# Kernel optimization log

Hardware: AMD Instinct MI355X
Metric: run time of the kernel (lower is better)

The kernel has to match this reference:

```python
import jax, jax.numpy as jnp
import numpy as np

EPS = 1e-6
NUM_HEADS = 16


def layer_norm(x, a, b):
    # Faithful to the custom LayerNorm: unbiased std (ddof=1), eps added to sigma.
    mu = jnp.mean(x, axis=-1, keepdims=True)
    sigma = jnp.std(x, axis=-1, keepdims=True, ddof=1) + EPS
    return (x - mu) / sigma * a + b


def entmax15(x):
    # Exact 1.5-entmax along the last axis (Peters et al. 2019, sort-based).
    S = x.shape[-1]
    x = x / 2.0
    x = x - jnp.max(x, axis=-1, keepdims=True)  # shift-invariant stabilization
    xs = jnp.flip(jnp.sort(x, axis=-1), axis=-1)  # descending
    k = jnp.arange(1, S + 1, dtype=x.dtype)
    mean = jnp.cumsum(xs, axis=-1) / k
    meansq = jnp.cumsum(xs * xs, axis=-1) / k
    ss = k * (meansq - mean * mean)
    delta = (1.0 - ss) / k
    tau = mean - jnp.sqrt(jnp.clip(delta, 0.0))
    support_size = jnp.sum((tau <= xs).astype(jnp.int32), axis=-1, keepdims=True)
    tau_star = jnp.take_along_axis(tau, support_size - 1, axis=-1)
    return jnp.clip(x - tau_star, 0.0) ** 2


def linear(x, w, b):
    return jnp.einsum('bsd,od->bso', x, w) + b


def setup_inputs() -> dict:
    key = jax.random.key(0)
    B, S, D, DFF = 1, 2048, 1024, 4096
    ks = jax.random.split(key, 12)
    p = lambda k, shape: jax.random.normal(k, shape, dtype=jnp.float32) * 0.02
    return {
        'inputs': jax.random.normal(ks[0], (B, S, D), dtype=jnp.float32),
        'mask': jax.random.randint(ks[1], (B, S), 0, 2, dtype=jnp.int32),
        'wq': p(ks[2], (D, D)), 'bq': jnp.zeros((D,), jnp.float32),
        'wk': p(ks[3], (D, D)), 'bk': jnp.zeros((D,), jnp.float32),
        'wv': p(ks[4], (D, D)), 'bv': jnp.zeros((D,), jnp.float32),
        'wo': p(ks[5], (D, D)), 'bo': jnp.zeros((D,), jnp.float32),
        'ln1_a': jnp.ones((D,), jnp.float32), 'ln1_b': jnp.zeros((D,), jnp.float32),
        'w1': p(ks[6], (DFF, D)), 'b1': jnp.zeros((DFF,), jnp.float32),
        'w2': p(ks[7], (D, DFF)), 'b2': jnp.zeros((D,), jnp.float32),
        'ln2_a': jnp.ones((D,), jnp.float32), 'ln2_b': jnp.zeros((D,), jnp.float32),
    }


def reference(inputs, mask, wq, bq, wk, bk, wv, bv, wo, bo, ln1_a, ln1_b,
              w1, b1, w2, b2, ln2_a, ln2_b):
    B, S, D = inputs.shape
    H = NUM_HEADS
    hd = D // H

    # --- Sublayer 1: pre-norm -> SparseMHA -> residual (dropout=0 -> identity) ---
    x1 = layer_norm(inputs, ln1_a, ln1_b)
    split = lambda t: t.reshape(B, S, H, hd).transpose(0, 2, 1, 3)  # [B,H,S,hd]
    q = split(linear(x1, wq, bq))
    k = split(linear(x1, wk, bk))
    v = split(linear(x1, wv, bv))

    scores = jnp.einsum('bhqd,bhkd->bhqk', q, k) / jnp.sqrt(jnp.asarray(hd, jnp.float32))
    # torch: mask.unsqueeze(0) -> (1,B,S); with B==1 it broadcasts as a key mask (1,1,1,S)
    mask4 = mask[None, None]  # (1,1,B,S), B==1
    scores = jnp.where(mask4 == 0, jnp.float32(-1e9), scores)

    p_attn = entmax15(scores).astype(jnp.float32)
    attended = jnp.einsum('bhqk,bhkd->bhqd', p_attn, v)
    attended = attended.transpose(0, 2, 1, 3).reshape(B, S, D)
    y = inputs + linear(attended, wo, bo)

    # --- Sublayer 2: pre-norm -> FFN -> residual ---
    x2 = layer_norm(y, ln2_a, ln2_b)
    ffn = linear(jax.nn.relu(linear(x2, w1, b1)), w2, b2)
    return y + ffn
```

## Files before the change

### kernel.cpp

```cpp
#include <hip/hip_runtime.h>
#include <hip/hip_bf16.h>

#define S   2048
#define D   1024
#define DFF 4096
#define NH  16
#define HD  64

typedef unsigned short u16;
typedef unsigned int   u32;
typedef __attribute__((ext_vector_type(8))) short      short8;
typedef __attribute__((ext_vector_type(4))) float      floatx4;
typedef __attribute__((ext_vector_type(2))) _Float16   half2v;
typedef __attribute__((ext_vector_type(4))) _Float16   half4v;
typedef __attribute__((ext_vector_type(8))) _Float16   half8v;

__device__ __forceinline__ float bu2f(u16 u) {
    union { u32 i; float f; } x; x.i = ((u32)u) << 16; return x.f;
}
__device__ __forceinline__ u16 f2bu(float f) {
    __hip_bfloat16 h = __float2bfloat16(f);
    return *(u16*)&h;
}
__device__ __forceinline__ u16 f2h(float f) {
    _Float16 h = (_Float16)f; return *(u16*)&h;
}
__device__ __forceinline__ float ldf(const float* p) { return *p; }
__device__ __forceinline__ float ldf(const u16* p)   { return bu2f(*p); }

__device__ __forceinline__ half2v pkrtz(float a, float b) {
    auto v = __builtin_amdgcn_cvt_pkrtz(a, b);
    union { decltype(v) i; half2v o; } u; u.i = v; return u.o;
}

__device__ __forceinline__ floatx4 mfma_f16(half8v a, half8v b, floatx4 c) {
    return __builtin_amdgcn_mfma_f32_16x16x32_f16(a, b, c, 0, 0, 0);
}
__device__ __forceinline__ float fdot2f(half2v a, half2v b, float c) {
#if __has_builtin(__builtin_amdgcn_fdot2)
    return __builtin_amdgcn_fdot2(a, b, c, false);
#else
    return c + (float)a[0] * (float)b[0] + (float)a[1] * (float)b[1];
#endif
}

template <int K>
__device__ __forceinline__ float ror16f(float v) {
    int s = __builtin_bit_cast(int, v);
    int r = __builtin_amdgcn_update_dpp(s, s, 0x120 | K, 0xF, 0xF, false);
    return __builtin_bit_cast(float, r);
}
__device__ __forceinline__ float rowsum16(float v) {
    v += ror16f<1>(v);
    v += ror16f<2>(v);
    v += ror16f<4>(v);
    v += ror16f<8>(v);
    return v;
}
__device__ __forceinline__ float rowmax16(float v) {
    v = fmaxf(v, ror16f<1>(v));
    v = fmaxf(v, ror16f<2>(v));
    v = fmaxf(v, ror16f<4>(v));
    v = fmaxf(v, ror16f<8>(v));
    return v;
}

__device__ __forceinline__ void async16(const void* g, void* l) {
    __builtin_amdgcn_global_load_lds(
        (const __attribute__((address_space(1))) u32*)g,
        (__attribute__((address_space(3))) u32*)l, 16, 0, 0);
}

#define WAITV(N) asm volatile("s_waitcnt vmcnt(" N ")" ::: "memory")
#define WAITL()  asm volatile("s_waitcnt lgkmcnt(0)" ::: "memory")
#define SBAR()   __builtin_amdgcn_s_barrier()
#define SCHED0() __builtin_amdgcn_sched_barrier(0)

__global__ __launch_bounds__(256)
void cvt_kernel(const float* __restrict__ in, u16* __restrict__ out, int n4)
{
    int i = blockIdx.x * 256 + threadIdx.x;
    if (i < n4) {
        float4 v = ((const float4*)in)[i];
        ushort4 s;
        s.x = f2bu(v.x); s.y = f2bu(v.y); s.z = f2bu(v.z); s.w = f2bu(v.w);
        ((ushort4*)out)[i] = s;
    }
}

__global__ __launch_bounds__(256)
void prep_kernel(const int* __restrict__ mask, int* __restrict__ newpos,
                 int* __restrict__ nkbuf,
                 const float* __restrict__ wq, const float* __restrict__ wk,
                 const float* __restrict__ wv, const float* __restrict__ wo,
                 u16* __restrict__ wqkvb, u16* __restrict__ wob,
                 const float* __restrict__ inp, const float* __restrict__ ln1a,
                 const float* __restrict__ ln1b, u16* __restrict__ x1,
                 const float* __restrict__ w2, u16* __restrict__ w2dst)
{
    const int blk = blockIdx.x;
    const int t = threadIdx.x;
    if (blk == 0) {
        __shared__ int ps[256];
        int loc[8];
        int s = 0;
#pragma unroll
        for (int j = 0; j < 8; j++) {
            loc[j] = s;
            s += (mask[t * 8 + j] != 0);
        }
        ps[t] = s;
        __syncthreads();
        for (int off = 1; off < 256; off <<= 1) {
            int v = (t >= off) ? ps[t - off] : 0;
            __syncthreads();
            ps[t] += v;
            __syncthreads();
        }
        const int total = ps[255];
        const int base = t ? ps[t - 1] : 0;
#pragma unroll
        for (int j = 0; j < 8; j++) {
            const int gi = t * 8 + j;
            const int up = base + loc[j];
            newpos[gi] = mask[gi] ? up : (total + gi - up);
        }
        if (t == 0) nkbuf[0] = total;
    } else if (blk <= 4096) {
        int cb = blk - 1;
        const float* src;
        u16* dst;
        if (cb < 1024)      { src = wq; dst = wqkvb; }
        else if (cb < 2048) { src = wk; dst = wqkvb + 1024 * 1024; cb -= 1024; }
        else if (cb < 3072) { src = wv; dst = wqkvb + 2 * 1024 * 1024; cb -= 2048; }
        else                { src = wo; dst = wob; cb -= 3072; }
        const int i = cb * 256 + t;
        float4 v = ((const float4*)src)[i];
        ushort4 sv;
        sv.x = f2bu(v.x); sv.y = f2bu(v.y); sv.z = f2bu(v.z); sv.w = f2bu(v.w);
        ((ushort4*)dst)[i] = sv;
    } else if (blk <= 6144) {
        const int rrow = blk - 4097;
        const float* x = inp + (size_t)rrow * D;
        float v[4];
        float s = 0.f, ss = 0.f;
#pragma unroll
        for (int j = 0; j < 4; j++) {
            float val = x[t + 256 * j];
            v[j] = val; s += val; ss = fmaf(val, val, ss);
        }
#pragma unroll
        for (int off = 32; off >= 1; off >>= 1) {
            s  += __shfl_down(s,  off, 64);
            ss += __shfl_down(ss, off, 64);
        }
        __shared__ float red[10];
        const int wave = t >> 6, lane = t & 63;
        if (lane == 0) { red[wave] = s; red[4 + wave] = ss; }
        __syncthreads();
        if (t == 0) {
            float S1 = red[0] + red[1] + red[2] + red[3];
            float S2 = red[4] + red[5] + red[6] + red[7];
            float mu = S1 / (float)D;
            float var = (S2 - (float)D * mu * mu) / (float)(D - 1);
            float sig = sqrtf(fmaxf(var, 0.f)) + 1e-6f;
            red[8] = mu; red[9] = 1.f / sig;
        }
        __syncthreads();
        const float mu = red[8], rs = red[9];
#pragma unroll
        for (int j = 0; j < 4; j++) {
            int c = t + 256 * j;
            x1[(size_t)rrow * D + c] = f2bu((v[j] - mu) * rs * ln1a[c] + ln1b[c]);
        }
    } else {
        const int i = (blk - 6145) * 256 + t;
        float4 v = ((const float4*)w2)[i];
        ushort4 sv;
        sv.x = f2bu(v.x); sv.y = f2bu(v.y); sv.z = f2bu(v.z); sv.w = f2bu(v.w);
        ((ushort4*)w2dst)[i] = sv;
    }
}

template <typename T>
__global__ __launch_bounds__(256, 4)
void ln_kernel(const T* __restrict__ in, const float* __restrict__ ga,
               const float* __restrict__ gb, u16* __restrict__ out)
{
    const int row = blockIdx.x;
    const int t = threadIdx.x;
    const T* x = in + (size_t)row * D;
    float v[4];
    float s = 0.f, ss = 0.f;
#pragma unroll
    for (int j = 0; j < 4; j++) {
        float val = ldf(x + t + 256 * j);
        v[j] = val; s += val; ss = fmaf(val, val, ss);
    }
#pragma unroll
    for (int off = 32; off >= 1; off >>= 1) {
        s  += __shfl_down(s,  off, 64);
        ss += __shfl_down(ss, off, 64);
    }
    __shared__ float red[10];
    const int wave = t >> 6, lane = t & 63;
    if (lane == 0) { red[wave] = s; red[4 + wave] = ss; }
    __syncthreads();
    if (t == 0) {
        float S1 = red[0] + red[1] + red[2] + red[3];
        float S2 = red[4] + red[5] + red[6] + red[7];
        float mu = S1 / (float)D;
        float var = (S2 - (float)D * mu * mu) / (float)(D - 1);
        float sig = sqrtf(fmaxf(var, 0.f)) + 1e-6f;
        red[8] = mu; red[9] = 1.f / sig;
    }
    __syncthreads();
    const float mu = red[8], rs = red[9];
#pragma unroll
    for (int j = 0; j < 4; j++) {
        int c = t + 256 * j;
        out[(size_t)row * D + c] = f2bu((v[j] - mu) * rs * ga[c] + gb[c]);
    }
}

#define GEMM_CORE(A_, B_, K_)                                                   \
    __shared__ u16 As[3 * 128 * 32];                                            \
    __shared__ u16 Bs[3 * 128 * 32];                                            \
    const int t = threadIdx.x;                                                  \
    const int w = t >> 6, l = t & 63;                                           \
    const int m0 = blockIdx.y * 128, n0 = blockIdx.x * 128;                     \
    const int qk = l >> 4, col = l & 15;                                        \
    const int wm = (w & 1) * 64, wn = (w >> 1) * 64;                            \
    const int sr  = l >> 2;                                                     \
    const int sq  = l & 3;                                                      \
    const int row = w * 16 + sr;                                                \
    const int gq  = sq ^ ((row >> 1) & 3);                                      \
    const u16* Ap = A_ + (size_t)(m0 + row) * K_ + gq * 8;                      \
    const u16* Bp = B_ + (size_t)(n0 + row) * K_ + gq * 8;                      \
    u16* AsW = As + w * 16 * 32;                                                \
    u16* BsW = Bs + w * 16 * 32;                                                \
    const int mloc = wm + col, nloc = wn + col;                                 \
    const int aoff = mloc * 32 + (qk ^ ((mloc >> 1) & 3)) * 8;                  \
    const int boff = nloc * 32 + (qk ^ ((nloc >> 1) & 3)) * 8;                  \
    floatx4 acc[4][4];                                                          \
    _Pragma("unroll")                                                           \
    for (int i = 0; i < 4; i++)                                                 \
        _Pragma("unroll")                                                       \
        for (int j = 0; j < 4; j++) acc[i][j] = (floatx4)0.f;                   \
    const int NT_ = K_ / 32;                                                    \
    _Pragma("unroll")                                                           \
    for (int s = 0; s < 3; s++) {                                               \
        async16(Ap,                   AsW + s * 4096);                          \
        async16(Ap + (size_t)64 * K_, AsW + s * 4096 + 64 * 32);                \
        async16(Bp,                   BsW + s * 4096);                          \
        async16(Bp + (size_t)64 * K_, BsW + s * 4096 + 64 * 32);                \
        Ap += 32; Bp += 32;                                                     \
    }                                                                           \
    WAITV("8"); SCHED0(); SBAR();                                               \
    int cur = 0;                                                                \
    for (int t0 = 0; t0 + 3 < NT_; ++t0) {                                      \
        short8 a[4], b[4];                                                      \
        const u16* aB = As + cur * 4096 + aoff;                                 \
        const u16* bB = Bs + cur * 4096 + boff;                                 \
        _Pragma("unroll")                                                       \
        for (int i = 0; i < 4; i++) a[i] = *(const short8*)(aB + i * 16 * 32);  \
        _Pragma("unroll")                                                       \
        for (int j = 0; j < 4; j++) b[j] = *(const short8*)(bB + j * 16 * 32);  \
        WAITL(); SCHED0(); SBAR();                                              \
        async16(Ap,                   AsW + cur * 4096);                        \
        async16(Ap + (size_t)64 * K_, AsW + cur * 4096 + 64 * 32);              \
        async16(Bp,                   BsW + cur * 4096);                        \
        async16(Bp + (size_t)64 * K_, BsW + cur * 4096 + 64 * 32);              \
        Ap += 32; Bp += 32;                                                     \
        _Pragma("unroll")                                                       \
        for (int i = 0; i < 4; i++)                                             \
            _Pragma("unroll")                                                   \
            for (int j = 0; j < 4; j++)                                         \
                acc[i][j] = __builtin_amdgcn_mfma_f32_16x16x32_bf16(            \
                    a[i], b[j], acc[i][j], 0, 0, 0);                            \
        WAITV("8"); SCHED0(); SBAR();                                           \
        cur = cur + 1; if (cur == 3) cur = 0;                                   \
    }                                                                           \
    _Pragma("unroll")                                                           \
    for (int tail = 0; tail < 3; tail++) {                                      \
        short8 a[4], b[4];                                                      \
        const u16* aB = As + cur * 4096 + aoff;                                 \
        const u16* bB = Bs + cur * 4096 + boff;                                 \
        _Pragma("unroll")                                                       \
        for (int i = 0; i < 4; i++) a[i] = *(const short8*)(aB + i * 16 * 32);  \
        _Pragma("unroll")                                                       \
        for (int j = 0; j < 4; j++) b[j] = *(const short8*)(bB + j * 16 * 32);  \
        _Pragma("unroll")                                                       \
        for (int i = 0; i < 4; i++)                                             \
            _Pragma("unroll")                                                   \
            for (int j = 0; j < 4; j++)                                         \
                acc[i][j] = __builtin_amdgcn_mfma_f32_16x16x32_bf16(            \
                    a[i], b[j], acc[i][j], 0, 0, 0);                            \
        if (tail == 0) { WAITV("4"); SCHED0(); SBAR(); }                        \
        if (tail == 1) { WAITV("0"); SCHED0(); SBAR(); }                        \
        cur = cur + 1; if (cur == 3) cur = 0;                                   \
    }

template <int OMODE, bool RELU, int RES>
__global__ __launch_bounds__(256, 2)
void gemm_mfma(const u16* __restrict__ A, const u16* __restrict__ B,
               const float* __restrict__ bias, const void* __restrict__ res,
               void* __restrict__ Cout, int M, int N, int K)
{
    GEMM_CORE(A, B, K)
#pragma unroll
    for (int j = 0; j < 4; j++) {
        const int n = n0 + wn + j * 16 + col;
        const float bn = bias[n];
#pragma unroll
        for (int i = 0; i < 4; i++) {
#pragma unroll
            for (int r = 0; r < 4; r++) {
                const int m = m0 + wm + i * 16 + qk * 4 + r;
                float v = acc[i][j][r] + bn;
                if (RELU) v = fmaxf(v, 0.f);
                if (RES == 1) v += ((const float*)res)[(size_t)m * N + n];
                if (RES == 2) v += bu2f(((const u16*)res)[(size_t)m * N + n]);
                if (OMODE == 0) ((float*)Cout)[(size_t)m * N + n] = v;
                if (OMODE == 1) ((u16*)Cout)[(size_t)m * N + n] = f2bu(v);
            }
        }
    }
}

__global__ __launch_bounds__(256, 2)
void gemm_qkv(const u16* __restrict__ A, const u16* __restrict__ B,
              const float* __restrict__ bq, const float* __restrict__ bk,
              const float* __restrict__ bv, const int* __restrict__ np,
              u16* __restrict__ outQ, u16* __restrict__ outK,
              u16* __restrict__ outVT)
{
    const int K = D;
    GEMM_CORE(A, B, K)
    const int seg   = n0 >> 10;
    const int nbase = n0 & 1023;
    const float* bs = (seg == 0) ? bq : (seg == 1) ? bk : bv;
    int npm[4][4];
    if (seg != 0) {
#pragma unroll
        for (int i = 0; i < 4; i++)
#pragma unroll
            for (int r = 0; r < 4; r++)
                npm[i][r] = np[m0 + wm + i * 16 + qk * 4 + r];
    }
#pragma unroll
    for (int j = 0; j < 4; j++) {
        const int nl = nbase + wn + j * 16 + col;
        const float bn = bs[nl];
#pragma unroll
        for (int i = 0; i < 4; i++) {
#pragma unroll
            for (int r = 0; r < 4; r++) {
                const int m = m0 + wm + i * 16 + qk * 4 + r;
                float v = acc[i][j][r] + bn;
                if (seg == 0)      outQ [(size_t)m * D + nl]          = f2h(v);
                else if (seg == 1) outK [(size_t)npm[i][r] * D + nl]  = f2h(v);
                else               outVT[(size_t)nl * S + npm[i][r]]  = f2h(v);
            }
        }
    }
}

template <int OMODE, int RES>
__global__ __launch_bounds__(256, 4)
void gemm64(const u16* __restrict__ A, const u16* __restrict__ B,
            const float* __restrict__ bias, const void* __restrict__ res,
            void* __restrict__ Cout, int M, int N, int K)
{
    __shared__ u16 As[3 * 64 * 32];
    __shared__ u16 Bs[3 * 64 * 32];
    const int t = threadIdx.x;
    const int w = t >> 6, l = t & 63;
    const int m0 = blockIdx.y * 64, n0 = blockIdx.x * 64;
    const int qk = l >> 4, col = l & 15;
    const int wm = (w & 1) * 32, wn = (w >> 1) * 32;
    const int sr = l >> 2, sq = l & 3;
    const int row = w * 16 + sr;
    const int gq = sq ^ ((row >> 1) & 3);
    const u16* Ap = A + (size_t)(m0 + row) * K + gq * 8;
    const u16* Bp = B + (size_t)(n0 + row) * K + gq * 8;
    u16* AsW = As + w * 16 * 32;
    u16* BsW = Bs + w * 16 * 32;
    const int mloc = wm + col, nloc = wn + col;
    const int aoff = mloc * 32 + (qk ^ ((mloc >> 1) & 3)) * 8;
    const int boff = nloc * 32 + (qk ^ ((nloc >> 1) & 3)) * 8;
    floatx4 acc[2][2];
#pragma unroll
    for (int i = 0; i < 2; i++)
#pragma unroll
        for (int j = 0; j < 2; j++) acc[i][j] = (floatx4)0.f;
    const int NT_ = K / 32;
#pragma unroll
    for (int s = 0; s < 3; s++) {
        async16(Ap, AsW + s * 2048);
        async16(Bp, BsW + s * 2048);
        Ap += 32; Bp += 32;
    }
    WAITV("4"); SCHED0(); SBAR();
    int cur = 0;
    for (int t0 = 0; t0 + 3 < NT_; ++t0) {
        short8 a[2], b[2];
        const u16* aB = As + cur * 2048 + aoff;
        const u16* bB = Bs + cur * 2048 + boff;
#pragma unroll
        for (int i = 0; i < 2; i++) a[i] = *(const short8*)(aB + i * 16 * 32);
#pragma unroll
        for (int j = 0; j < 2; j++) b[j] = *(const short8*)(bB + j * 16 * 32);
        WAITL(); SCHED0(); SBAR();
        async16(Ap, AsW + cur * 2048);
        async16(Bp, BsW + cur * 2048);
        Ap += 32; Bp += 32;
#pragma unroll
        for (int i = 0; i < 2; i++)
#pragma unroll
            for (int j = 0; j < 2; j++)
                acc[i][j] = __builtin_amdgcn_mfma_f32_16x16x32_bf16(
                    a[i], b[j], acc[i][j], 0, 0, 0);
        WAITV("4"); SCHED0(); SBAR();
        cur = cur + 1; if (cur == 3) cur = 0;
    }
#pragma unroll
    for (int tail = 0; tail < 3; tail++) {
        short8 a[2], b[2];
        const u16* aB = As + cur * 2048 + aoff;
        const u16* bB = Bs + cur * 2048 + boff;
#pragma unroll
        for (int i = 0; i < 2; i++) a[i] = *(const short8*)(aB + i * 16 * 32);
#pragma unroll
        for (int j = 0; j < 2; j++) b[j] = *(const short8*)(bB + j * 16 * 32);
#pragma unroll
        for (int i = 0; i < 2; i++)
#pragma unroll
            for (int j = 0; j < 2; j++)
                acc[i][j] = __builtin_amdgcn_mfma_f32_16x16x32_bf16(
                    a[i], b[j], acc[i][j], 0, 0, 0);
        if (tail == 0) { WAITV("2"); SCHED0(); SBAR(); }
        if (tail == 1) { WAITV("0"); SCHED0(); SBAR(); }
        cur = cur + 1; if (cur == 3) cur = 0;
    }
#pragma unroll
    for (int j = 0; j < 2; j++) {
        const int n = n0 + wn + j * 16 + col;
        const float bn = bias[n];
#pragma unroll
        for (int i = 0; i < 2; i++) {
#pragma unroll
            for (int r = 0; r < 4; r++) {
                const int m = m0 + wm + i * 16 + qk * 4 + r;
                float v = acc[i][j][r] + bn;
                if (RES == 1) v += ((const float*)res)[(size_t)m * N + n];
                if (RES == 2) v += bu2f(((const u16*)res)[(size_t)m * N + n]);
                if (OMODE == 0) ((float*)Cout)[(size_t)m * N + n] = v;
                if (OMODE == 1) ((u16*)Cout)[(size_t)m * N + n] = f2bu(v);
            }
        }
    }
}

__global__ __launch_bounds__(256, 3)
void attn_cvt(const u16* __restrict__ qb, const u16* __restrict__ kb,
              const u16* __restrict__ vT, const int* __restrict__ nkbuf,
              u16* __restrict__ att,
              const float* __restrict__ w1src, u16* __restrict__ w1dst)
{
    __shared__ u16 Plds[16 * 1024];
    const int blk = blockIdx.x;
    const int t  = threadIdx.x;
    if (blk >= 2048) {
        const int i = (blk - 2048) * 256 + t;
        float4 v = ((const float4*)w1src)[i];
        ushort4 sv;
        sv.x = f2bu(v.x); sv.y = f2bu(v.y); sv.z = f2bu(v.z); sv.w = f2bu(v.w);
        ((ushort4*)w1dst)[i] = sv;
        return;
    }
    const int nk = nkbuf[0];
    const int NS = (nk + 127) >> 7;
    const int NT = (nk + 31) >> 5;
    const int hh = blk >> 7;
    const int q0 = (blk & 127) * 16;
    const int w  = __builtin_amdgcn_readfirstlane(t >> 6);
    const int l  = t & 63;
    const int lg = l >> 4, lc = l & 15;
    const _Float16 NEG = (_Float16)(-30000.f);
    const half4v NEG4 = {NEG, NEG, NEG, NEG};

    const u16* qp = qb + (size_t)(q0 + lc) * D + hh * HD + lg * 8;
    const half8v bq0 = *(const half8v*)qp;
    const half8v bq1 = *(const half8v*)(qp + 32);
    const u16* kbase = kb + hh * HD + lg * 8;
    const int R = 4 * w + lg;
    const half2v one2 = {(_Float16)1.f, (_Float16)1.f};
    const u16* vp = vT + (size_t)(hh * HD + w * 16 + lc) * S + lg * 8;

    if (nk <= 1152) {
#pragma unroll
        for (int T = 0; T < 16; T++) {
            const int g = 4 * T + w;
            if (g < 8 * NS) {
                half4v scv;
                if ((g + 1) * 16 <= nk) {
                    const u16* kp = kbase + (size_t)(g * 16 + lc) * D;
                    floatx4 a = (floatx4)0.f;
                    a = mfma_f16(*(const half8v*)kp,        bq0, a);
                    a = mfma_f16(*(const half8v*)(kp + 32), bq1, a);
                    half2v p01 = pkrtz(a[0] * 0.0625f, a[1] * 0.0625f);
                    half2v p23 = pkrtz(a[2] * 0.0625f, a[3] * 0.0625f);
                    scv = __builtin_shufflevector(p01, p23, 0, 1, 2, 3);
                } else if (g * 16 < nk) {
                    const u16* kp = kbase + (size_t)(g * 16 + lc) * D;
                    floatx4 a = (floatx4)0.f;
                    a = mfma_f16(*(const half8v*)kp,        bq0, a);
                    a = mfma_f16(*(const half8v*)(kp + 32), bq1, a);
                    const int kb0 = g * 16 + lg * 4;
                    half2v p01 = pkrtz(kb0 + 0 < nk ? a[0] * 0.0625f : -30000.f,
                                       kb0 + 1 < nk ? a[1] * 0.0625f : -30000.f);
                    half2v p23 = pkrtz(kb0 + 2 < nk ? a[2] * 0.0625f : -30000.f,
                                       kb0 + 3 < nk ? a[3] * 0.0625f : -30000.f);
                    scv = __builtin_shufflevector(p01, p23, 0, 1, 2, 3);
                } else {
                    scv = NEG4;
                }
                const int kl = g * 16 + lg * 4;
                const int b  = kl >> 3;
                const int p  = b ^ ((b >> 3) & 7) ^ (lc & 7);
                *(half4v*)&Plds[lc * 1024 + p * 8 + (lg & 1) * 4] = scv;
            }
        }
        __syncthreads();

        half8v xq[9];
#pragma unroll
        for (int s = 0; s < 8; s++) {
            if (s < NS) {
                const int b = 16 * s + lc;
                const int p = b ^ ((b >> 3) & 7) ^ (R & 7);
                xq[s] = *(const half8v*)&Plds[R * 1024 + p * 8];
            }
        }
        if (NS > 8) {
            __syncthreads();
#pragma unroll
            for (int T = 16; T < 18; T++) {
                const int g = 4 * T + w;
                half4v scv;
                if ((g + 1) * 16 <= nk) {
                    const u16* kp = kbase + (size_t)(g * 16 + lc) * D;
                    floatx4 a = (floatx4)0.f;
                    a = mfma_f16(*(const half8v*)kp,        bq0, a);
                    a = mfma_f16(*(const half8v*)(kp + 32), bq1, a);
                    half2v p01 = pkrtz(a[0] * 0.0625f, a[1] * 0.0625f);
                    half2v p23 = pkrtz(a[2] * 0.0625f, a[3] * 0.0625f);
                    scv = __builtin_shufflevector(p01, p23, 0, 1, 2, 3);
                } else if (g * 16 < nk) {
                    const u16* kp = kbase + (size_t)(g * 16 + lc) * D;
                    floatx4 a = (floatx4)0.f;
                    a = mfma_f16(*(const half8v*)kp,        bq0, a);
                    a = mfma_f16(*(const half8v*)(kp + 32), bq1, a);
                    const int kb0 = g * 16 + lg * 4;
                    half2v p01 = pkrtz(kb0 + 0 < nk ? a[0] * 0.0625f : -30000.f,
                                       kb0 + 1 < nk ? a[1] * 0.0625f : -30000.f);
                    half2v p23 = pkrtz(kb0 + 2 < nk ? a[2] * 0.0625f : -30000.f,
                                       kb0 + 3 < nk ? a[3] * 0.0625f : -30000.f);
                    scv = __builtin_shufflevector(p01, p23, 0, 1, 2, 3);
                } else {
                    scv = NEG4;
                }
                const int kl = g * 16 + lg * 4 - 1024;
                const int b  = kl >> 3;
                const int p  = b ^ ((b >> 3) & 7) ^ (lc & 7);
                *(half4v*)&Plds[lc * 1024 + p * 8 + (lg & 1) * 4] = scv;
            }
            __syncthreads();
            {
                const int b = lc;
                const int p = b ^ ((b >> 3) & 7) ^ (R & 7);
                xq[8] = *(const half8v*)&Plds[R * 1024 + p * 8];
            }
        }

        float tau;
        {
            half8v m8 = xq[0];
#pragma unroll
            for (int i = 1; i < 9; i++)
                if (i < NS) m8 = __builtin_elementwise_max(m8, xq[i]);
            union { half8v v; half2v h[4]; } u; u.v = m8;
            half2v m2 = __builtin_elementwise_max(
                __builtin_elementwise_max(u.h[0], u.h[1]),
                __builtin_elementwise_max(u.h[2], u.h[3]));
            float mx = fmaxf((float)m2[0], (float)m2[1]);
            mx = rowmax16(mx);
            tau = mx - 1.0f;
        }

        const float nact = (float)(8 * NS);
#pragma unroll 1
        for (int it = 0; it < 12; it++) {
            const _Float16 th = (_Float16)tau;
            const float tf = (float)th;
            const half8v t8 = {th, th, th, th, th, th, th, th};
            float m1a = 0.f, m1b = 0.f, m2a = 0.f, m2b = 0.f;
#pragma unroll
            for (int i = 0; i < 9; i++) {
                if (i < NS) {
                    union { half8v v; half2v h[4]; } u;
                    u.v = __builtin_elementwise_max(xq[i], t8);
                    m1a = fdot2f(u.h[0], one2, m1a);
                    m2a = fdot2f(u.h[0], u.h[0], m2a);
                    m1b = fdot2f(u.h[1], one2, m1b);
                    m2b = fdot2f(u.h[1], u.h[1], m2b);
                    m1a = fdot2f(u.h[2], one2, m1a);
                    m2a = fdot2f(u.h[2], u.h[2], m2a);
                    m1b = fdot2f(u.h[3], one2, m1b);
                    m2b = fdot2f(u.h[3], u.h[3], m2b);
                }
            }
            const float M1 = m1a + m1b, M2 = m2a + m2b;
            float s1 = fmaf(-nact, tf, M1);
            float s2 = fmaf(tf, fmaf(nact, tf, -2.f * M1), M2);
            s1 = rowsum16(s1);
            s2 = rowsum16(s2);
            const float delta = (s2 - 1.0f) / (2.0f * fmaxf(s1, 1e-4f));
            tau += delta;
            if (__all(fabsf(delta) < 2.5e-4f)) break;
        }

        const _Float16 th = (_Float16)tau;
        const half8v t8 = {th, th, th, th, th, th, th, th};
        const half8v z8 = (half8v)(_Float16)0.f;
        floatx4 oa0 = (floatx4)0.f, oa1 = (floatx4)0.f;
        floatx4 oa2 = (floatx4)0.f, oa3 = (floatx4)0.f;
#pragma unroll
        for (int s = 0; s < 8; s++) {
            if (s < NS) {
                half8v dp = __builtin_elementwise_max(xq[s] - t8, z8);
                const int b = 16 * s + lc;
                const int p = b ^ ((b >> 3) & 7) ^ (R & 7);
                *(half8v*)&Plds[R * 1024 + p * 8] = dp * dp;
            }
        }
        __syncthreads();
        __builtin_amdgcn_s_setprio(1);
#pragma unroll
        for (int kt = 0; kt < 32; kt++) {
            if (kt < NT) {
                const int b = kt * 4 + lg;
                const int p = b ^ ((b >> 3) & 7) ^ (lc & 7);
                half8v af = *(const half8v*)&Plds[lc * 1024 + p * 8];
                half8v bf = *(const half8v*)(vp + kt * 32);
                if ((kt & 3) == 0)      oa0 = mfma_f16(af, bf, oa0);
                else if ((kt & 3) == 1) oa1 = mfma_f16(af, bf, oa1);
                else if ((kt & 3) == 2) oa2 = mfma_f16(af, bf, oa2);
                else                    oa3 = mfma_f16(af, bf, oa3);
            }
        }
        __builtin_amdgcn_s_setprio(0);
        if (NS > 8) {
            __syncthreads();
            {
                half8v dp = __builtin_elementwise_max(xq[8] - t8, z8);
                const int b = lc;
                const int p = b ^ ((b >> 3) & 7) ^ (R & 7);
                *(half8v*)&Plds[R * 1024 + p * 8] = dp * dp;
            }
            __syncthreads();
            const u16* vph = vp + 1024;
#pragma unroll
            for (int kt2 = 0; kt2 < 4; kt2++) {
                if (32 + kt2 < NT) {
                    const int b = kt2 * 4 + lg;
                    const int p = b ^ ((b >> 3) & 7) ^ (lc & 7);
                    half8v af = *(const half8v*)&Plds[lc * 1024 + p * 8];
                    half8v bf = *(const half8v*)(vph + kt2 * 32);
                    if ((kt2 & 3) == 0)      oa0 = mfma_f16(af, bf, oa0);
                    else if ((kt2 & 3) == 1) oa1 = mfma_f16(af, bf, oa1);
                    else if ((kt2 & 3) == 2) oa2 = mfma_f16(af, bf, oa2);
                    else                     oa3 = mfma_f16(af, bf, oa3);
                }
            }
        }
        const floatx4 oacc = (oa0 + oa1) + (oa2 + oa3);
#pragma unroll
        for (int r = 0; r < 4; r++)
            att[(size_t)(q0 + lg * 4 + r) * D + hh * HD + w * 16 + lc] =
                f2bu(oacc[r]);
    } else {
        half4v sc[32];
        {
            __builtin_amdgcn_s_setprio(1);
#pragma unroll
            for (int T = 0; T < 32; T++) {
                const int g = 4 * T + w;
                if (g * 16 < nk) {
                    const u16* kp = kbase + (size_t)(g * 16 + lc) * D;
                    floatx4 a = (floatx4)0.f;
                    a = mfma_f16(*(const half8v*)kp,        bq0, a);
                    a = mfma_f16(*(const half8v*)(kp + 32), bq1, a);
                    const int kb0 = g * 16 + lg * 4;
                    half2v p01 = pkrtz(kb0 + 0 < nk ? a[0] * 0.0625f : -30000.f,
                                       kb0 + 1 < nk ? a[1] * 0.0625f : -30000.f);
                    half2v p23 = pkrtz(kb0 + 2 < nk ? a[2] * 0.0625f : -30000.f,
                                       kb0 + 3 < nk ? a[3] * 0.0625f : -30000.f);
                    sc[T] = __builtin_shufflevector(p01, p23, 0, 1, 2, 3);
                } else {
                    sc[T] = NEG4;
                }
            }
            __builtin_amdgcn_s_setprio(0);
        }

        half8v xq[16];
        {
#pragma unroll
            for (int T = 0; T < 16; T++) {
                const int g  = 4 * T + w;
                const int kl = g * 16 + lg * 4;
                const int b  = kl >> 3;
                const int p  = b ^ ((b >> 3) & 7) ^ (lc & 7);
                *(half4v*)&Plds[lc * 1024 + p * 8 + (lg & 1) * 4] = sc[T];
            }
            __syncthreads();
#pragma unroll
            for (int s = 0; s < 8; s++) {
                if (s < NS) {
                    const int b = 16 * s + lc;
                    const int p = b ^ ((b >> 3) & 7) ^ (R & 7);
                    xq[s] = *(const half8v*)&Plds[R * 1024 + p * 8];
                }
            }
            __syncthreads();
#pragma unroll
            for (int T = 16; T < 32; T++) {
                const int g  = 4 * T + w;
                const int kl = g * 16 + lg * 4 - 1024;
                const int b  = kl >> 3;
                const int p  = b ^ ((b >> 3) & 7) ^ (lc & 7);
                *(half4v*)&Plds[lc * 1024 + p * 8 + (lg & 1) * 4] = sc[T];
            }
            __syncthreads();
#pragma unroll
            for (int s = 0; s < 8; s++) {
                const int j = 8 + s;
                if (j < NS) {
                    const int b = 16 * s + lc;
                    const int p = b ^ ((b >> 3) & 7) ^ (R & 7);
                    xq[j] = *(const half8v*)&Plds[R * 1024 + p * 8];
                }
            }
        }

        float tau;
        {
            half8v m8 = xq[0];
#pragma unroll
            for (int i = 1; i < 16; i++)
                if (i < NS) m8 = __builtin_elementwise_max(m8, xq[i]);
            union { half8v v; half2v h[4]; } u; u.v = m8;
            half2v m2 = __builtin_elementwise_max(
                __builtin_elementwise_max(u.h[0], u.h[1]),
                __builtin_elementwise_max(u.h[2], u.h[3]));
            float mx = fmaxf((float)m2[0], (float)m2[1]);
            mx = rowmax16(mx);
            tau = mx - 1.0f;
        }

        const float nact = (float)(8 * NS);
#pragma unroll 1
        for (int it = 0; it < 12; it++) {
            const _Float16 th = (_Float16)tau;
            const float tf = (float)th;
            const half8v t8 = {th, th, th, th, th, th, th, th};
            float m1a = 0.f, m1b = 0.f, m2a = 0.f, m2b = 0.f;
#pragma unroll
            for (int i = 0; i < 16; i++) {
                if (i < NS) {
                    union { half8v v; half2v h[4]; } u;
                    u.v = __builtin_elementwise_max(xq[i], t8);
                    m1a = fdot2f(u.h[0], one2, m1a);
                    m2a = fdot2f(u.h[0], u.h[0], m2a);
                    m1b = fdot2f(u.h[1], one2, m1b);
                    m2b = fdot2f(u.h[1], u.h[1], m2b);
                    m1a = fdot2f(u.h[2], one2, m1a);
                    m2a = fdot2f(u.h[2], u.h[2], m2a);
                    m1b = fdot2f(u.h[3], one2, m1b);
                    m2b = fdot2f(u.h[3], u.h[3], m2b);
                }
            }
            const float M1 = m1a + m1b, M2 = m2a + m2b;
            float s1 = fmaf(-nact, tf, M1);
            float s2 = fmaf(tf, fmaf(nact, tf, -2.f * M1), M2);
            s1 = rowsum16(s1);
            s2 = rowsum16(s2);
            const float delta = (s2 - 1.0f) / (2.0f * fmaxf(s1, 1e-4f));
            tau += delta;
            if (__all(fabsf(delta) < 2.5e-4f)) break;
        }

        const _Float16 th = (_Float16)tau;
        const half8v t8 = {th, th, th, th, th, th, th, th};
        const half8v z8 = (half8v)(_Float16)0.f;
        floatx4 oa0 = (floatx4)0.f, oa1 = (floatx4)0.f;
        floatx4 oa2 = (floatx4)0.f, oa3 = (floatx4)0.f;
#pragma unroll
        for (int s = 0; s < 8; s++) {
            if (s < NS) {
                half8v dp = __builtin_elementwise_max(xq[s] - t8, z8);
                const int b = 16 * s + lc;
                const int p = b ^ ((b >> 3) & 7) ^ (R & 7);
                *(half8v*)&Plds[R * 1024 + p * 8] = dp * dp;
            }
        }
        __syncthreads();
        __builtin_amdgcn_s_setprio(1);
#pragma unroll
        for (int kt = 0; kt < 32; kt++) {
            if (kt < NT) {
                const int b = kt * 4 + lg;
                const int p = b ^ ((b >> 3) & 7) ^ (lc & 7);
                half8v af = *(const half8v*)&Plds[lc * 1024 + p * 8];
                half8v bf = *(const half8v*)(vp + kt * 32);
                if ((kt & 3) == 0)      oa0 = mfma_f16(af, bf, oa0);
                else if ((kt & 3) == 1) oa1 = mfma_f16(af, bf, oa1);
                else if ((kt & 3) == 2) oa2 = mfma_f16(af, bf, oa2);
                else                    oa3 = mfma_f16(af, bf, oa3);
            }
        }
        __builtin_amdgcn_s_setprio(0);
        {
            __syncthreads();
#pragma unroll
            for (int s = 0; s < 8; s++) {
                const int j = 8 + s;
                if (j < NS) {
                    half8v dp = __builtin_elementwise_max(xq[j] - t8, z8);
                    const int b = 16 * s + lc;
                    const int p = b ^ ((b >> 3) & 7) ^ (R & 7);
                    *(half8v*)&Plds[R * 1024 + p * 8] = dp * dp;
                }
            }
            __syncthreads();
            const u16* vph = vp + 1024;
            __builtin_amdgcn_s_setprio(1);
#pragma unroll
            for (int kt = 0; kt < 32; kt++) {
                if (32 + kt < NT) {
                    const int b = kt * 4 + lg;
                    const int p = b ^ ((b >> 3) & 7) ^ (lc & 7);
                    half8v af = *(const half8v*)&Plds[lc * 1024 + p * 8];
                    half8v bf = *(const half8v*)(vph + kt * 32);
                    if ((kt & 3) == 0)      oa0 = mfma_f16(af, bf, oa0);
                    else if ((kt & 3) == 1) oa1 = mfma_f16(af, bf, oa1);
                    else if ((kt & 3) == 2) oa2 = mfma_f16(af, bf, oa2);
                    else                    oa3 = mfma_f16(af, bf, oa3);
                }
            }
            __builtin_amdgcn_s_setprio(0);
        }
        const floatx4 oacc = (oa0 + oa1) + (oa2 + oa3);
#pragma unroll
        for (int r = 0; r < 4; r++)
            att[(size_t)(q0 + lg * 4 + r) * D + hh * HD + w * 16 + lc] =
                f2bu(oacc[r]);
    }
}

extern "C" void kernel_launch(void* const* d_in, const int* in_sizes, int n_in,
                              void* d_out, int out_size, void* d_ws, size_t ws_size,
                              hipStream_t stream)
{
    const float* inp  = (const float*)d_in[0];
    const int*   mask = (const int*)d_in[1];
    const float* wq   = (const float*)d_in[2];
    const float* bq   = (const float*)d_in[3];
    const float* wk   = (const float*)d_in[4];
    const float* bk   = (const float*)d_in[5];
    const float* wv   = (const float*)d_in[6];
    const float* bv   = (const float*)d_in[7];
    const float* wo   = (const float*)d_in[8];
    const float* bo   = (const float*)d_in[9];
    const float* ln1a = (const float*)d_in[10];
    const float* ln1b = (const float*)d_in[11];
    const float* w1   = (const float*)d_in[12];
    const float* b1   = (const float*)d_in[13];
    const float* w2   = (const float*)d_in[14];
    const float* b2   = (const float*)d_in[15];
    const float* ln2a = (const float*)d_in[16];
    const float* ln2b = (const float*)d_in[17];

    const size_t MB = 1u << 20;
    char* w = (char*)d_ws;
    u16* wqkvb = (u16*)(w + 0 * MB);
    u16* w1b   = (u16*)(w + 0 * MB);
    u16* x1    = (u16*)(w + 8 * MB);
    u16* att   = x1;
    u16* x2    = x1;
    u16* qb_   = (u16*)(w + 12 * MB);
    u16* yb    = (u16*)(w + 12 * MB);
    u16* kb_   = (u16*)(w + 16 * MB);
    u16* vTb   = (u16*)(w + 20 * MB);
    u16* wob   = (u16*)(w + 24 * MB);
    u16* hb    = (u16*)(w + 16 * MB);
    int* np    = (int*)(w + 26 * MB);
    int* nkbuf = np + 2048;
    float* outF = (float*)d_out;

    const bool w2early = (ws_size >= 40 * MB);
    u16* w2b = w2early ? (u16*)(w + 32 * MB) : (u16*)(w + 0 * MB);

    prep_kernel<<<w2early ? 10241 : 6145, 256, 0, stream>>>(
        mask, np, nkbuf, wq, wk, wv, wo, wqkvb, wob,
        inp, ln1a, ln1b, x1, w2, w2b);
    gemm_qkv<<<dim3(3 * D / 128, S / 128), 256, 0, stream>>>(
        x1, wqkvb, bq, bk, bv, np, qb_, kb_, vTb);
    attn_cvt<<<2048 + 4096, 256, 0, stream>>>(qb_, kb_, vTb, nkbuf, att,
                                              w1, w1b);
    gemm64<1, 1><<<dim3(D / 64, S / 64), 256, 0, stream>>>(
        att, wob, bo, inp, yb, S, D, D);
    ln_kernel<u16><<<S, 256, 0, stream>>>(yb, ln2a, ln2b, x2);
    gemm_mfma<1, true, 0><<<dim3(DFF / 128, S / 128), 256, 0, stream>>>(
        x2, w1b, b1, nullptr, hb, S, DFF, D);
    if (!w2early)
        cvt_kernel<<<4096, 256, 0, stream>>>(w2, w2b, (DFF * D) / 4);
    gemm64<0, 2><<<dim3(D / 64, S / 64), 256, 0, stream>>>(
        hb, w2b, b2, yb, outF, S, D, DFF);
}
```

Measured before the change: 314.9 us.

## Switch QKV projection to 64x64 tiles and raise GEMM occupancy bounds

Replaces the 128x128-tile QKV GEMM with a 64x64-tile variant built from a shared GEMM64 core macro, giving four times as many blocks (1536 vs 384) so more of the GPU is busy. It also raises launch_bounds min-blocks for gemm_mfma (2→3) and gemm64 (4→6), pushing the compiler to limit registers for higher occupancy. Smaller tiles mean less data reuse per block and more global/LDS traffic, and tighter register limits risk spills.

```diff
diff --git a/kernel.cpp b/kernel.cpp
--- a/kernel.cpp
+++ b/kernel.cpp
@@ -302,7 +302,7 @@
     }
 
 template <int OMODE, bool RELU, int RES>
-__global__ __launch_bounds__(256, 2)
+__global__ __launch_bounds__(256, 3)
 void gemm_mfma(const u16* __restrict__ A, const u16* __restrict__ B,
                const float* __restrict__ bias, const void* __restrict__ res,
                void* __restrict__ Cout, int M, int N, int K)
@@ -328,121 +328,86 @@
     }
 }
 
-__global__ __launch_bounds__(256, 2)
-void gemm_qkv(const u16* __restrict__ A, const u16* __restrict__ B,
-              const float* __restrict__ bq, const float* __restrict__ bk,
-              const float* __restrict__ bv, const int* __restrict__ np,
-              u16* __restrict__ outQ, u16* __restrict__ outK,
-              u16* __restrict__ outVT)
-{
-    const int K = D;
-    GEMM_CORE(A, B, K)
-    const int seg   = n0 >> 10;
-    const int nbase = n0 & 1023;
-    const float* bs = (seg == 0) ? bq : (seg == 1) ? bk : bv;
-    int npm[4][4];
-    if (seg != 0) {
-#pragma unroll
-        for (int i = 0; i < 4; i++)
-#pragma unroll
-            for (int r = 0; r < 4; r++)
-                npm[i][r] = np[m0 + wm + i * 16 + qk * 4 + r];
-    }
-#pragma unroll
-    for (int j = 0; j < 4; j++) {
-        const int nl = nbase + wn + j * 16 + col;
-        const float bn = bs[nl];
-#pragma unroll
-        for (int i = 0; i < 4; i++) {
-#pragma unroll
-            for (int r = 0; r < 4; r++) {
-                const int m = m0 + wm + i * 16 + qk * 4 + r;
-                float v = acc[i][j][r] + bn;
-                if (seg == 0)      outQ [(size_t)m * D + nl]          = f2h(v);
-                else if (seg == 1) outK [(size_t)npm[i][r] * D + nl]  = f2h(v);
-                else               outVT[(size_t)nl * S + npm[i][r]]  = f2h(v);
-            }
-        }
-    }
-}
+#define GEMM64_CORE(A_, B_, K_, N0MUL)                                          \
+    __shared__ u16 As[3 * 64 * 32];                                             \
+    __shared__ u16 Bs[3 * 64 * 32];                                             \
+    const int t = threadIdx.x;                                                  \
+    const int w = t >> 6, l = t & 63;                                           \
+    const int m0 = blockIdx.y * 64, n0 = blockIdx.x * N0MUL;                    \
+    const int qk = l >> 4, col = l & 15;                                        \
+    const int wm = (w & 1) * 32, wn = (w >> 1) * 32;                            \
+    const int sr = l >> 2, sq = l & 3;                                          \
+    const int row = w * 16 + sr;                                                \
+    const int gq = sq ^ ((row >> 1) & 3);                                       \
+    const u16* Ap = A_ + (size_t)(m0 + row) * K_ + gq * 8;                      \
+    const u16* Bp = B_ + (size_t)(n0 + row) * K_ + gq * 8;                      \
+    u16* AsW = As + w * 16 * 32;                                                \
+    u16* BsW = Bs + w * 16 * 32;                                                \
+    const int mloc = wm + col, nloc = wn + col;                                 \
+    const int aoff = mloc * 32 + (qk ^ ((mloc >> 1) & 3)) * 8;                  \
+    const int boff = nloc * 32 + (qk ^ ((nloc >> 1) & 3)) * 8;                  \
+    floatx4 acc[2][2];                                                          \
+    _Pragma("unroll")                                                           \
+    for (int i = 0; i < 2; i++)                                                 \
+        _Pragma("unroll")                                                       \
+        for (int j = 0; j < 2; j++) acc[i][j] = (floatx4)0.f;                   \
+    const int NT_ = K_ / 32;                                                    \
+    _Pragma("unroll")                                                           \
+    for (int s = 0; s < 3; s++) {                                               \
+        async16(Ap, AsW + s * 2048);                                            \
+        async16(Bp, BsW + s * 2048);                                            \
+        Ap += 32; Bp += 32;                                                     \
+    }                                                                           \
+    WAITV("4"); SCHED0(); SBAR();                                               \
+    int cur = 0;                                                                \
+    for (int t0 = 0; t0 + 3 < NT_; ++t0) {                                      \
+        short8 a[2], b[2];                                                      \
+        const u16* aB = As + cur * 2048 + aoff;                                 \
+        const u16* bB = Bs + cur * 2048 + boff;                                 \
+        _Pragma("unroll")                                                       \
+        for (int i = 0; i < 2; i++) a[i] = *(const short8*)(aB + i * 16 * 32);  \
+        _Pragma("unroll")                                                       \
+        for (int j = 0; j < 2; j++) b[j] = *(const short8*)(bB + j * 16 * 32);  \
+        WAITL(); SCHED0(); SBAR();                                              \
+        async16(Ap, AsW + cur * 2048);                                          \
+        async16(Bp, BsW + cur * 2048);                                          \
+        Ap += 32; Bp += 32;                                                     \
+        _Pragma("unroll")                                                       \
+        for (int i = 0; i < 2; i++)                                             \
+            _Pragma("unroll")                                                   \
+            for (int j = 0; j < 2; j++)                                         \
+                acc[i][j] = __builtin_amdgcn_mfma_f32_16x16x32_bf16(            \
+                    a[i], b[j], acc[i][j], 0, 0, 0);                            \
+        WAITV("4"); SCHED0(); SBAR();                                           \
+        cur = cur + 1; if (cur == 3) cur = 0;                                   \
+    }                                                                           \
+    _Pragma("unroll")                                                           \
+    for (int tail = 0; tail < 3; tail++) {                                      \
+        short8 a[2], b[2];                                                      \
+        const u16* aB = As + cur * 2048 + aoff;                                 \
+        const u16* bB = Bs + cur * 2048 + boff;                                 \
+        _Pragma("unroll")                                                       \
+        for (int i = 0; i < 2; i++) a[i] = *(const short8*)(aB + i * 16 * 32);  \
+        _Pragma("unroll")                                                       \
+        for (int j = 0; j < 2; j++) b[j] = *(const short8*)(bB + j * 16 * 32);  \
+        _Pragma("unroll")                                                       \
+        for (int i = 0; i < 2; i++)                                             \
+            _Pragma("unroll")                                                   \
+            for (int j = 0; j < 2; j++)                                         \
+                acc[i][j] = __builtin_amdgcn_mfma_f32_16x16x32_bf16(            \
+                    a[i], b[j], acc[i][j], 0, 0, 0);                            \
+        if (tail == 0) { WAITV("2"); SCHED0(); SBAR(); }                        \
+        if (tail == 1) { WAITV("0"); SCHED0(); SBAR(); }                        \
+        cur = cur + 1; if (cur == 3) cur = 0;                                   \
+    }
 
 template <int OMODE, int RES>
-__global__ __launch_bounds__(256, 4)
+__global__ __launch_bounds__(256, 6)
 void gemm64(const u16* __restrict__ A, const u16* __restrict__ B,
             const float* __restrict__ bias, const void* __restrict__ res,
             void* __restrict__ Cout, int M, int N, int K)
 {
-    __shared__ u16 As[3 * 64 * 32];
-    __shared__ u16 Bs[3 * 64 * 32];
-    const int t = threadIdx.x;
-    const int w = t >> 6, l = t & 63;
-    const int m0 = blockIdx.y * 64, n0 = blockIdx.x * 64;
-    const int qk = l >> 4, col = l & 15;
-    const int wm = (w & 1) * 32, wn = (w >> 1) * 32;
-    const int sr = l >> 2, sq = l & 3;
-    const int row = w * 16 + sr;
-    const int gq = sq ^ ((row >> 1) & 3);
-    const u16* Ap = A + (size_t)(m0 + row) * K + gq * 8;
-    const u16* Bp = B + (size_t)(n0 + row) * K + gq * 8;
-    u16* AsW = As + w * 16 * 32;
-    u16* BsW = Bs + w * 16 * 32;
-    const int mloc = wm + col, nloc = wn + col;
-    const int aoff = mloc * 32 + (qk ^ ((mloc >> 1) & 3)) * 8;
-    const int boff = nloc * 32 + (qk ^ ((nloc >> 1) & 3)) * 8;
-    floatx4 acc[2][2];
-#pragma unroll
-    for (int i = 0; i < 2; i++)
-#pragma unroll
-        for (int j = 0; j < 2; j++) acc[i][j] = (floatx4)0.f;
-    const int NT_ = K / 32;
-#pragma unroll
-    for (int s = 0; s < 3; s++) {
-        async16(Ap, AsW + s * 2048);
-        async16(Bp, BsW + s * 2048);
-        Ap += 32; Bp += 32;
-    }
-    WAITV("4"); SCHED0(); SBAR();
-    int cur = 0;
-    for (int t0 = 0; t0 + 3 < NT_; ++t0) {
-        short8 a[2], b[2];
-        const u16* aB = As + cur * 2048 + aoff;
-        const u16* bB = Bs + cur * 2048 + boff;
-#pragma unroll
-        for (int i = 0; i < 2; i++) a[i] = *(const short8*)(aB + i * 16 * 32);
-#pragma unroll
-        for (int j = 0; j < 2; j++) b[j] = *(const short8*)(bB + j * 16 * 32);
-        WAITL(); SCHED0(); SBAR();
-        async16(Ap, AsW + cur * 2048);
-        async16(Bp, BsW + cur * 2048);
-        Ap += 32; Bp += 32;
-#pragma unroll
-        for (int i = 0; i < 2; i++)
-#pragma unroll
-            for (int j = 0; j < 2; j++)
-                acc[i][j] = __builtin_amdgcn_mfma_f32_16x16x32_bf16(
-                    a[i], b[j], acc[i][j], 0, 0, 0);
-        WAITV("4"); SCHED0(); SBAR();
-        cur = cur + 1; if (cur == 3) cur = 0;
-    }
-#pragma unroll
-    for (int tail = 0; tail < 3; tail++) {
-        short8 a[2], b[2];
-        const u16* aB = As + cur * 2048 + aoff;
-        const u16* bB = Bs + cur * 2048 + boff;
-#pragma unroll
-        for (int i = 0; i < 2; i++) a[i] = *(const short8*)(aB + i * 16 * 32);
-#pragma unroll
-        for (int j = 0; j < 2; j++) b[j] = *(const short8*)(bB + j * 16 * 32);
-#pragma unroll
-        for (int i = 0; i < 2; i++)
-#pragma unroll
-            for (int j = 0; j < 2; j++)
-                acc[i][j] = __builtin_amdgcn_mfma_f32_16x16x32_bf16(
-                    a[i], b[j], acc[i][j], 0, 0, 0);
-        if (tail == 0) { WAITV("2"); SCHED0(); SBAR(); }
-        if (tail == 1) { WAITV("0"); SCHED0(); SBAR(); }
-        cur = cur + 1; if (cur == 3) cur = 0;
-    }
+    GEMM64_CORE(A, B, K, 64)
 #pragma unroll
     for (int j = 0; j < 2; j++) {
         const int n = n0 + wn + j * 16 + col;
@@ -457,6 +422,43 @@
                 if (RES == 2) v += bu2f(((const u16*)res)[(size_t)m * N + n]);
                 if (OMODE == 0) ((float*)Cout)[(size_t)m * N + n] = v;
                 if (OMODE == 1) ((u16*)Cout)[(size_t)m * N + n] = f2bu(v);
+            }
+        }
+    }
+}
+
+__global__ __launch_bounds__(256, 6)
+void gemm64_qkv(const u16* __restrict__ A, const u16* __restrict__ B,
+                const float* __restrict__ bq, const float* __restrict__ bk,
+                const float* __restrict__ bv, const int* __restrict__ np,
+                u16* __restrict__ outQ, u16* __restrict__ outK,
+                u16* __restrict__ outVT)
+{
+    GEMM64_CORE(A, B, D, 64)
+    const int seg   = n0 >> 10;
+    const int nbase = n0 & 1023;
+    const float* bs = (seg == 0) ? bq : (seg == 1) ? bk : bv;
+    int npm[2][4];
+    if (seg != 0) {
+#pragma unroll
+        for (int i = 0; i < 2; i++)
+#pragma unroll
+            for (int r = 0; r < 4; r++)
+                npm[i][r] = np[m0 + wm + i * 16 + qk * 4 + r];
+    }
+#pragma unroll
+    for (int j = 0; j < 2; j++) {
+        const int nl = nbase + wn + j * 16 + col;
+        const float bn = bs[nl];
+#pragma unroll
+        for (int i = 0; i < 2; i++) {
+#pragma unroll
+            for (int r = 0; r < 4; r++) {
+                const int m = m0 + wm + i * 16 + qk * 4 + r;
+                float v = acc[i][j][r] + bn;
+                if (seg == 0)      outQ [(size_t)m * D + nl]          = f2h(v);
+                else if (seg == 1) outK [(size_t)npm[i][r] * D + nl]  = f2h(v);
+                else               outVT[(size_t)nl * S + npm[i][r]]  = f2h(v);
             }
         }
     }
@@ -916,7 +918,7 @@
     prep_kernel<<<w2early ? 10241 : 6145, 256, 0, stream>>>(
         mask, np, nkbuf, wq, wk, wv, wo, wqkvb, wob,
         inp, ln1a, ln1b, x1, w2, w2b);
-    gemm_qkv<<<dim3(3 * D / 128, S / 128), 256, 0, stream>>>(
+    gemm64_qkv<<<dim3(3 * D / 64, S / 64), 256, 0, stream>>>(
         x1, wqkvb, bq, bk, bv, np, qb_, kb_, vTb);
     attn_cvt<<<2048 + 4096, 256, 0, stream>>>(qb_, kb_, vTb, nkbuf, att,
                                               w1, w1b);
```

After: 317.0 us. Within noise of the previous version (+0.7%).
